# Kernel optimization log

Measured on AMD Instinct MI355X. Metric: run time of the kernel, lower is better.

## Reference

```python
import jax, jax.numpy as jnp
import numpy as np

V, T, D, H, L, F, B = 50257, 1024, 1024, 16, 10, 4096, 2
HD = D // H  # head_dim = 64
EPS = 1e-5


def sinusoidal_pos(seq_len, d_model):
    pos = np.arange(seq_len)[:, None].astype(np.float32)
    i = np.arange(d_model // 2).astype(np.float32)
    inv = 1.0 / (10000.0 ** (2.0 * i / d_model))
    ang = pos * inv[None, :]
    pe = np.zeros((seq_len, d_model), dtype=np.float32)
    pe[:, 0::2] = np.sin(ang)
    pe[:, 1::2] = np.cos(ang)
    return jnp.asarray(pe)


def setup_inputs() -> dict:
    key = jax.random.key(0)
    ks = jax.random.split(key, 16)
    s = 0.02
    return {
        "x": jax.random.randint(ks[0], (B, T), 0, V),
        "emb": jax.random.normal(ks[1], (V, D), jnp.float32) * s,
        "pos": sinusoidal_pos(T, D),
        "Wq": jax.random.normal(ks[2], (L, D, D), jnp.float32) * s,
        "bq": jnp.zeros((L, D), jnp.float32),
        "Wk": jax.random.normal(ks[3], (L, D, D), jnp.float32) * s,
        "bk": jnp.zeros((L, D), jnp.float32),
        "Wv": jax.random.normal(ks[4], (L, D, D), jnp.float32) * s,
        "bv": jnp.zeros((L, D), jnp.float32),
        "ln_g": jnp.ones((L, D), jnp.float32),
        "ln_b": jnp.zeros((L, D), jnp.float32),
        "W1": jax.random.normal(ks[5], (L, D, F), jnp.float32) * s,
        "b1": jnp.zeros((L, F), jnp.float32),
        "W2": jax.random.normal(ks[6], (L, F, D), jnp.float32) * s,
        "b2": jnp.zeros((L, D), jnp.float32),
        "lnf_g": jnp.ones((D,), jnp.float32),
        "lnf_b": jnp.zeros((D,), jnp.float32),
        "Wout": jax.random.normal(ks[7], (D, V), jnp.float32) * s,
        "bout": jnp.zeros((V,), jnp.float32),
    }


def layer_norm(h, g, b):
    mu = jnp.mean(h, axis=-1, keepdims=True)
    var = jnp.mean(jnp.square(h - mu), axis=-1, keepdims=True)
    return (h - mu) * jax.lax.rsqrt(var + EPS) * g + b


def reference(x, emb, pos, Wq, bq, Wk, bk, Wv, bv, ln_g, ln_b, W1, b1, W2, b2, lnf_g, lnf_b, Wout, bout):
    t = x.shape[1]
    h = emb[x] + pos[None, :t]  # [B,T,D]
    causal = jnp.tril(jnp.ones((t, t), bool))  # True = keep
    scale = 1.0 / jnp.sqrt(jnp.float32(HD))

    def body(h, p):
        wq, bq_, wk, bk_, wv, bv_, g, bln, w1, b1_, w2, b2_ = p
        q = (h @ wq + bq_).reshape(B, t, H, HD)
        k = (h @ wk + bk_).reshape(B, t, H, HD)
        v = (h @ wv + bv_).reshape(B, t, H, HD)
        score = jnp.einsum('bqhd,bkhd->bhqk', q, k) * scale
        score = jnp.where(causal, score, -jnp.inf)
        attn = jax.nn.softmax(score, axis=-1)
        o = jnp.einsum('bhqk,bkhd->bqhd', attn, v).reshape(B, t, D)
        h = layer_norm(h + o, g, bln)
        m = jax.nn.gelu(h @ w1 + b1_, approximate=False) @ w2 + b2_
        h = layer_norm(h + m, g, bln)  # same LayerNorm params reused, as in source
        return h, None

    h, _ = jax.lax.scan(body, h, (Wq, bq, Wk, bk, Wv, bv, ln_g, ln_b, W1, b1, W2, b2))
    h = layer_norm(h, lnf_g, lnf_b)
    return h @ Wout + bout  # [B,T,V]
```

## Files before the change

### kernel.cpp

```cpp
#include <hip/hip_runtime.h>
#include <cstdint>
#include <cstddef>

#define Vv 50257
#define Va 50304
#define Tt 1024
#define Dd 1024
#define Hh 16
#define Ll 10
#define Ff 4096
#define Bb 2
#define Mm (Bb*Tt)

typedef float f32x4 __attribute__((ext_vector_type(4)));
typedef __bf16 bf16x8 __attribute__((ext_vector_type(8)));
typedef unsigned short u16x8 __attribute__((ext_vector_type(8)));
typedef unsigned short u16x4 __attribute__((ext_vector_type(4)));

static __device__ __forceinline__ unsigned short f2bf(float f) {
  unsigned int u = __builtin_bit_cast(unsigned int, f);
  unsigned int r = (u + 0x7FFFu + ((u >> 16) & 1u)) >> 16;
  return (unsigned short)r;
}

static __device__ __forceinline__ f32x4 mfma16x16x32(u16x8 a, u16x8 b, f32x4 c) {
  return __builtin_amdgcn_mfma_f32_16x16x32_bf16(
      __builtin_bit_cast(bf16x8, a), __builtin_bit_cast(bf16x8, b), c, 0, 0, 0);
}

static __device__ __forceinline__ void async_cp16(const void* g, void* l) {
  __builtin_amdgcn_global_load_lds(
      (const __attribute__((address_space(1))) unsigned int*)g,
      (__attribute__((address_space(3))) unsigned int*)l, 16, 0, 0);
}

__global__ __launch_bounds__(256) void embed_kernel(
    const int* __restrict__ x, const float* __restrict__ emb,
    const float* __restrict__ pos, float* __restrict__ h,
    unsigned short* __restrict__ hb) {
  int bt = blockIdx.x;
  int t = bt & (Tt - 1);
  int tok = x[bt];
  int i = threadIdx.x * 4;
  f32x4 e = *(const f32x4*)(emb + (size_t)tok * Dd + i);
  f32x4 p = *(const f32x4*)(pos + (size_t)t * Dd + i);
  f32x4 r = e + p;
  *(f32x4*)(h + (size_t)bt * Dd + i) = r;
  u16x4 rb = { f2bf(r[0]), f2bf(r[1]), f2bf(r[2]), f2bf(r[3]) };
  *(u16x4*)(hb + (size_t)bt * Dd + i) = rb;
}

__global__ __launch_bounds__(256) void add_ln_kernel(
    const float* __restrict__ hin, const float* __restrict__ r,
    const float* __restrict__ g, const float* __restrict__ bb,
    float* __restrict__ hout, unsigned short* __restrict__ hbout) {
  int row = blockIdx.x;
  int tid = threadIdx.x;
  size_t off = (size_t)row * Dd + tid * 4;
  f32x4 xv = *(const f32x4*)(hin + off);
  if (r) xv += *(const f32x4*)(r + off);
  float s  = xv[0] + xv[1] + xv[2] + xv[3];
  float ss = xv[0]*xv[0] + xv[1]*xv[1] + xv[2]*xv[2] + xv[3]*xv[3];
  #pragma unroll
  for (int o = 1; o < 64; o <<= 1) {
    s  += __shfl_xor(s, o);
    ss += __shfl_xor(ss, o);
  }
  __shared__ float red[8];
  int wave = tid >> 6, lane = tid & 63;
  if (lane == 0) { red[wave] = s; red[4 + wave] = ss; }
  __syncthreads();
  s  = red[0] + red[1] + red[2] + red[3];
  ss = red[4] + red[5] + red[6] + red[7];
  float mu = s * (1.0f / Dd);
  float var = ss * (1.0f / Dd) - mu * mu;
  float rstd = rsqrtf(var + 1e-5f);
  f32x4 gv = *(const f32x4*)(g + tid * 4);
  f32x4 bv = *(const f32x4*)(bb + tid * 4);
  f32x4 y;
  #pragma unroll
  for (int j = 0; j < 4; ++j) y[j] = (xv[j] - mu) * rstd * gv[j] + bv[j];
  *(f32x4*)(hout + off) = y;
  u16x4 yb = { f2bf(y[0]), f2bf(y[1]), f2bf(y[2]), f2bf(y[3]) };
  *(u16x4*)(hbout + off) = yb;
}

__global__ __launch_bounds__(256) void bias_gather_kernel(
    const float* __restrict__ bq, const float* __restrict__ bk,
    const float* __restrict__ bv, float* __restrict__ cb) {
  int l = blockIdx.x;
  int i = threadIdx.x * 4;
  f32x4 q = *(const f32x4*)(bq + (size_t)l * Dd + i);
  f32x4 k = *(const f32x4*)(bk + (size_t)l * Dd + i);
  f32x4 v = *(const f32x4*)(bv + (size_t)l * Dd + i);
  *(f32x4*)(cb + (size_t)l * 3072 + i) = q;
  *(f32x4*)(cb + (size_t)l * 3072 + 1024 + i) = k;
  *(f32x4*)(cb + (size_t)l * 3072 + 2048 + i) = v;
}

__global__ __launch_bounds__(256) void tconv_kernel(
    const float* __restrict__ W, unsigned short* __restrict__ Wt,
    int K, int N, int Nvalid, size_t sW, size_t sWt) {
  const float* Wl = W + (size_t)blockIdx.z * sW;
  unsigned short* Wtl = Wt + (size_t)blockIdx.z * sWt;
  __shared__ unsigned short t[64][72];
  int n0 = blockIdx.x * 64, k0 = blockIdx.y * 64;
  int tx = threadIdx.x & 15, ty = threadIdx.x >> 4;
  #pragma unroll
  for (int i = 0; i < 4; ++i) {
    int kr = ty + i * 16;
    int nc = tx * 4;
    int gn = n0 + nc;
    f32x4 v = {0.f, 0.f, 0.f, 0.f};
    if (gn + 3 < Nvalid) {
      v = *(const f32x4*)(Wl + (size_t)(k0 + kr) * N + gn);
    } else {
      #pragma unroll
      for (int j = 0; j < 4; ++j)
        if (gn + j < Nvalid) v[j] = Wl[(size_t)(k0 + kr) * N + gn + j];
    }
    t[nc + 0][kr] = f2bf(v[0]); t[nc + 1][kr] = f2bf(v[1]);
    t[nc + 2][kr] = f2bf(v[2]); t[nc + 3][kr] = f2bf(v[3]);
  }
  __syncthreads();
  #pragma unroll
  for (int i = 0; i < 4; ++i) {
    int nr = ty + i * 16;
    u16x4 o = *(const u16x4*)&t[nr][tx * 4];
    *(u16x4*)(Wtl + (size_t)(n0 + nr) * K + k0 + tx * 4) = o;
  }
}

template <int BM, int EPI>
__global__ __launch_bounds__(256) void gemm_bt(
    const unsigned short* __restrict__ A, const unsigned short* __restrict__ Bt,
    const float* __restrict__ bias, void* __restrict__ Cout,
    int Ncols, int K) {
  constexpr int NJ = (BM == 128) ? 4 : 2;
  __shared__ __align__(16) unsigned short Al[2][BM * 32];
  __shared__ __align__(16) unsigned short Bl[2][128 * 32];
  const int bm = blockIdx.x * BM;
  const int bn = blockIdx.y * 128;
  const int tid = threadIdx.x, lane = tid & 63, wave = tid >> 6;
  const int wm = (BM == 128) ? (wave >> 1) * 64 : 0;
  const int wn = (BM == 128) ? (wave & 1) * 64 : wave * 32;
  const int rowi = lane >> 2;
  const int koff = (lane & 3) * 8;

  auto stage = [&](int buf, int k0) {
    #pragma unroll
    for (int i = 0; i < BM / 64; ++i) {
      int ch = wave + i * 4;
      async_cp16(A + (size_t)(bm + ch * 16 + rowi) * K + k0 + koff, &Al[buf][ch * 512]);
    }
    #pragma unroll
    for (int i = 0; i < 2; ++i) {
      int ch = wave + i * 4;
      async_cp16(Bt + (size_t)(bn + ch * 16 + rowi) * K + k0 + koff, &Bl[buf][ch * 512]);
    }
  };

  f32x4 acc[4][NJ];
  #pragma unroll
  for (int i = 0; i < 4; ++i)
    #pragma unroll
    for (int j = 0; j < NJ; ++j) acc[i][j] = {0.f, 0.f, 0.f, 0.f};

  stage(0, 0);
  __syncthreads();
  int cur = 0;
  for (int k0 = 0; k0 < K; k0 += 32) {
    if (k0 + 32 < K) stage(cur ^ 1, k0 + 32);
    u16x8 af[4], bfr[NJ];
    #pragma unroll
    for (int i = 0; i < 4; ++i)
      af[i] = *(const u16x8*)&Al[cur][(wm + i * 16 + (lane & 15)) * 32 + (lane >> 4) * 8];
    #pragma unroll
    for (int j = 0; j < NJ; ++j)
      bfr[j] = *(const u16x8*)&Bl[cur][(wn + j * 16 + (lane & 15)) * 32 + (lane >> 4) * 8];
    #pragma unroll
    for (int i = 0; i < 4; ++i)
      #pragma unroll
      for (int j = 0; j < NJ; ++j)
        acc[i][j] = mfma16x16x32(af[i], bfr[j], acc[i][j]);
    __syncthreads();
    cur ^= 1;
  }

  #pragma unroll
  for (int j = 0; j < NJ; ++j) {
    int col = bn + wn + j * 16 + (lane & 15);
    bool cok = (col < Ncols);
    float bv = cok ? bias[col] : 0.0f;
    #pragma unroll
    for (int i = 0; i < 4; ++i) {
      #pragma unroll
      for (int rr = 0; rr < 4; ++rr) {
        int row = bm + wm + i * 16 + (lane >> 4) * 4 + rr;
        float val = acc[i][j][rr] + bv;
        if (cok) {
          if constexpr (EPI == 0) {
            ((float*)Cout)[(size_t)row * Ncols + col] = val;
          } else if constexpr (EPI == 1) {
            ((unsigned short*)Cout)[(size_t)row * Ncols + col] = f2bf(val);
          } else {
            float gv = 0.5f * val * (1.0f + erff(val * 0.70710678f));
            ((unsigned short*)Cout)[(size_t)row * Ncols + col] = f2bf(gv);
          }
        }
      }
    }
  }
}

template <int EPI>
__global__ __launch_bounds__(256) void gemm_f32b(
    const unsigned short* __restrict__ A, const float* __restrict__ Bw,
    const float* __restrict__ bias, void* __restrict__ Cout, int N, int K) {
  __shared__ __align__(16) unsigned short Al[128][40];
  __shared__ __align__(16) unsigned short Btl[128][40];
  const int bn = blockIdx.x * 128;
  const int bm = blockIdx.y * 128;
  const int tid = threadIdx.x;
  const int lane = tid & 63;
  const int wave = tid >> 6;
  const int wm = (wave >> 1) * 64;
  const int wn = (wave & 1) * 64;
  const bool nfast = ((N & 3) == 0);

  f32x4 acc[4][4];
  #pragma unroll
  for (int i = 0; i < 4; ++i)
    #pragma unroll
    for (int j = 0; j < 4; ++j) acc[i][j] = {0.f, 0.f, 0.f, 0.f};

  for (int k0 = 0; k0 < K; k0 += 32) {
    __syncthreads();
    #pragma unroll
    for (int i = 0; i < 2; ++i) {
      int c = tid + i * 256;
      int row = c >> 2, ko = (c & 3) * 8;
      u16x8 v = *(const u16x8*)(A + (size_t)(bm + row) * K + k0 + ko);
      *(u16x8*)&Al[row][ko] = v;
    }
    if (nfast) {
      #pragma unroll
      for (int i = 0; i < 4; ++i) {
        int c = tid + i * 256;
        int kr = c >> 5;
        int no = (c & 31) * 4;
        f32x4 v4 = *(const f32x4*)(Bw + (size_t)(k0 + kr) * N + bn + no);
        Btl[no + 0][kr] = f2bf(v4[0]); Btl[no + 1][kr] = f2bf(v4[1]);
        Btl[no + 2][kr] = f2bf(v4[2]); Btl[no + 3][kr] = f2bf(v4[3]);
      }
    } else {
      #pragma unroll
      for (int i = 0; i < 4; ++i) {
        int c = tid + i * 256;
        int kr = c >> 5;
        int nb = c & 31;
        #pragma unroll
        for (int j = 0; j < 4; ++j) {
          int col = nb + j * 32;
          float v = (bn + col < N) ? Bw[(size_t)(k0 + kr) * N + bn + col] : 0.0f;
          Btl[col][kr] = f2bf(v);
        }
      }
    }
    __syncthreads();
    u16x8 af[4], bfr[4];
    #pragma unroll
    for (int i = 0; i < 4; ++i)
      af[i] = *(const u16x8*)&Al[wm + i * 16 + (lane & 15)][(lane >> 4) * 8];
    #pragma unroll
    for (int j = 0; j < 4; ++j)
      bfr[j] = *(const u16x8*)&Btl[wn + j * 16 + (lane & 15)][(lane >> 4) * 8];
    #pragma unroll
    for (int i = 0; i < 4; ++i)
      #pragma unroll
      for (int j = 0; j < 4; ++j)
        acc[i][j] = mfma16x16x32(af[i], bfr[j], acc[i][j]);
  }
  #pragma unroll
  for (int j = 0; j < 4; ++j) {
    int col = bn + wn + j * 16 + (lane & 15);
    bool cok = (col < N);
    float bv = cok ? bias[col] : 0.0f;
    #pragma unroll
    for (int i = 0; i < 4; ++i) {
      #pragma unroll
      for (int rr = 0; rr < 4; ++rr) {
        int row = bm + wm + i * 16 + (lane >> 4) * 4 + rr;
        float val = acc[i][j][rr] + bv;
        if (cok) {
          if constexpr (EPI == 0) ((float*)Cout)[(size_t)row * N + col] = val;
          else if constexpr (EPI == 1) ((unsigned short*)Cout)[(size_t)row * N + col] = f2bf(val);
          else {
            float gv = 0.5f * val * (1.0f + erff(val * 0.70710678f));
            ((unsigned short*)Cout)[(size_t)row * N + col] = f2bf(gv);
          }
        }
      }
    }
  }
}

__global__ __launch_bounds__(256) void attn_kernel(
    const unsigned short* __restrict__ q, const unsigned short* __restrict__ k,
    const unsigned short* __restrict__ v, float* __restrict__ o, int ld) {
  const int ys = blockIdx.y;
  const int qt = (ys < 8) ? ys : 23 - ys;
  const int bh = blockIdx.x;
  const int b = bh >> 4, h = bh & 15;
  const size_t base = (size_t)b * Tt * ld + (size_t)h * 64;
  const int tid = threadIdx.x, lane = tid & 63, wave = tid >> 6;
  const int q0 = qt * 64 + wave * 16;

  __shared__ __align__(16) unsigned short Kl[64][72];
  __shared__ __align__(16) unsigned short Vt[64][72];
  __shared__ __align__(16) unsigned short Pl[4][16][72];

  const float SC = 0.18033688011112042f;

  u16x8 qa[2];
  {
    const unsigned short* qp = q + base + (size_t)(q0 + (lane & 15)) * ld + (lane >> 4) * 8;
    qa[0] = *(const u16x8*)qp;
    qa[1] = *(const u16x8*)(qp + 32);
  }

  f32x4 Oacc[4];
  #pragma unroll
  for (int df = 0; df < 4; ++df) Oacc[df] = {0.f, 0.f, 0.f, 0.f};
  float m_run[4], l_run[4];
  #pragma unroll
  for (int rr = 0; rr < 4; ++rr) { m_run[rr] = -__builtin_inff(); l_run[rr] = 0.f; }

  for (int kt = 0; kt <= qt; ++kt) {
    __syncthreads();
    #pragma unroll
    for (int i = 0; i < 2; ++i) {
      int c = tid + i * 256;
      int rr = c >> 3, dof = (c & 7) * 8;
      *(u16x8*)&Kl[rr][dof] =
          *(const u16x8*)(k + base + (size_t)(kt * 64 + rr) * ld + dof);
    }
    #pragma unroll
    for (int i = 0; i < 2; ++i) {
      int c = tid + i * 256;
      int rr = c >> 3, dof = (c & 7) * 8;
      u16x8 vv = *(const u16x8*)(v + base + (size_t)(kt * 64 + rr) * ld + dof);
      #pragma unroll
      for (int j = 0; j < 8; ++j) {
        int d = dof + j;
        Vt[d][(rr + (d & 56)) & 63] = vv[j];
      }
    }
    __syncthreads();

    f32x4 S[4];
    #pragma unroll
    for (int nf = 0; nf < 4; ++nf) {
      S[nf] = {0.f, 0.f, 0.f, 0.f};
      #pragma unroll
      for (int s = 0; s < 2; ++s) {
        u16x8 kb = *(const u16x8*)&Kl[nf * 16 + (lane & 15)][s * 32 + (lane >> 4) * 8];
        S[nf] = mfma16x16x32(qa[s], kb, S[nf]);
      }
    }
    const int kbase = kt * 64;
    float mx[4];
    #pragma unroll
    for (int rr = 0; rr < 4; ++rr) mx[rr] = -__builtin_inff();
    #pragma unroll
    for (int nf = 0; nf < 4; ++nf) {
      int kcol = kbase + nf * 16 + (lane & 15);
      #pragma unroll
      for (int rr = 0; rr < 4; ++rr) {
        int qrow = q0 + (lane >> 4) * 4 + rr;
        float sv = S[nf][rr] * SC;
        if (kcol > qrow) sv = -__builtin_inff();
        S[nf][rr] = sv;
        mx[rr] = fmaxf(mx[rr], sv);
      }
    }
    #pragma unroll
    for (int rr = 0; rr < 4; ++rr) {
      #pragma unroll
      for (int off = 1; off < 16; off <<= 1)
        mx[rr] = fmaxf(mx[rr], __shfl_xor(mx[rr], off));
    }
    float psum[4];
    #pragma unroll
    for (int rr = 0; rr < 4; ++rr) {
      float mnew = fmaxf(m_run[rr], mx[rr]);
      float sc = exp2f(m_run[rr] - mnew);
      l_run[rr] *= sc;
      #pragma unroll
      for (int df = 0; df < 4; ++df) Oacc[df][rr] *= sc;
      m_run[rr] = mnew;
      psum[rr] = 0.f;
    }
    #pragma unroll
    for (int nf = 0; nf < 4; ++nf) {
      #pragma unroll
      for (int rr = 0; rr < 4; ++rr) {
        float pv = exp2f(S[nf][rr] - m_run[rr]);
        S[nf][rr] = pv;
        psum[rr] += pv;
      }
    }
    #pragma unroll
    for (int rr = 0; rr < 4; ++rr) {
      #pragma unroll
      for (int off = 1; off < 16; off <<= 1) psum[rr] += __shfl_xor(psum[rr], off);
      l_run[rr] += psum[rr];
    }
    #pragma unroll
    for (int nf = 0; nf < 4; ++nf)
      #pragma unroll
      for (int rr = 0; rr < 4; ++rr)
        Pl[wave][(lane >> 4) * 4 + rr][nf * 16 + (lane & 15)] = f2bf(S[nf][rr]);
    __syncthreads();
    #pragma unroll
    for (int s = 0; s < 2; ++s) {
      u16x8 pa = *(const u16x8*)&Pl[wave][lane & 15][s * 32 + (lane >> 4) * 8];
      #pragma unroll
      for (int df = 0; df < 4; ++df) {
        int d = df * 16 + (lane & 15);
        int cs = (s * 32 + (lane >> 4) * 8 + (d & 56)) & 63;
        u16x8 vb = *(const u16x8*)&Vt[d][cs];
        Oacc[df] = mfma16x16x32(pa, vb, Oacc[df]);
      }
    }
  }

  #pragma unroll
  for (int df = 0; df < 4; ++df) {
    int d = df * 16 + (lane & 15);
    #pragma unroll
    for (int rr = 0; rr < 4; ++rr) {
      int qrow = q0 + (lane >> 4) * 4 + rr;
      o[((size_t)b * Tt + qrow) * Dd + h * 64 + d] = Oacc[df][rr] / l_run[rr];
    }
  }
}

extern "C" void kernel_launch(void* const* d_in, const int* in_sizes, int n_in,
                              void* d_out, int out_size, void* d_ws, size_t ws_size,
                              hipStream_t stream) {
  const int*   x     = (const int*)d_in[0];
  const float* emb   = (const float*)d_in[1];
  const float* pos   = (const float*)d_in[2];
  const float* Wq    = (const float*)d_in[3];
  const float* bq    = (const float*)d_in[4];
  const float* Wk    = (const float*)d_in[5];
  const float* bk    = (const float*)d_in[6];
  const float* Wv    = (const float*)d_in[7];
  const float* bv    = (const float*)d_in[8];
  const float* ln_g  = (const float*)d_in[9];
  const float* ln_b  = (const float*)d_in[10];
  const float* W1    = (const float*)d_in[11];
  const float* b1    = (const float*)d_in[12];
  const float* W2    = (const float*)d_in[13];
  const float* b2    = (const float*)d_in[14];
  const float* lnf_g = (const float*)d_in[15];
  const float* lnf_b = (const float*)d_in[16];
  const float* Wout  = (const float*)d_in[17];
  const float* bout  = (const float*)d_in[18];
  float* out = (float*)d_out;

  char* p = (char*)d_ws;
  auto alloc = [&](size_t bytes) {
    char* r = p; p += (bytes + 255) & ~(size_t)255; return r;
  };
  float* h           = (float*)alloc((size_t)Mm * Dd * 4);
  unsigned short* hb = (unsigned short*)alloc((size_t)Mm * Dd * 2);
  unsigned short* qkv = (unsigned short*)alloc((size_t)Mm * 3072 * 2);
  float* of          = (float*)alloc((size_t)Mm * Dd * 4);
  unsigned short* a1 = (unsigned short*)alloc((size_t)Mm * Ff * 2);
  float* cb          = (float*)alloc((size_t)Ll * 3072 * 4);
  size_t base_used = (size_t)(p - (char*)d_ws);

  const size_t SZ_WQKVT = (size_t)Ll * 3072 * Dd * 2;
  const size_t SZ_W1T   = (size_t)Ll * Ff * Dd * 2;
  const size_t SZ_W2T   = (size_t)Ll * Dd * Ff * 2;
  const size_t SZ_WOUTT = (size_t)Va * Dd * 2;
  const size_t need_big = base_used + SZ_WQKVT + SZ_W1T + SZ_W2T + SZ_WOUTT + 4096;
  const size_t need_rot = base_used + SZ_WOUTT + 4096;

  embed_kernel<<<Mm, 256, 0, stream>>>(x, emb, pos, h, hb);

  if (ws_size >= need_rot) {
    bias_gather_kernel<<<Ll, 256, 0, stream>>>(bq, bk, bv, cb);
    const bool big = (ws_size >= need_big);
    unsigned short *wqkvt, *w1t, *w2t, *woutt;
    if (big) {
      wqkvt = (unsigned short*)alloc(SZ_WQKVT);
      w1t   = (unsigned short*)alloc(SZ_W1T);
      w2t   = (unsigned short*)alloc(SZ_W2T);
      woutt = (unsigned short*)alloc(SZ_WOUTT);
      tconv_kernel<<<dim3(16, 16, Ll), 256, 0, stream>>>(
          Wq, wqkvt,           Dd, Dd, Dd, (size_t)Dd*Dd, (size_t)3072*Dd);
      tconv_kernel<<<dim3(16, 16, Ll), 256, 0, stream>>>(
          Wk, wqkvt + 1024*Dd, Dd, Dd, Dd, (size_t)Dd*Dd, (size_t)3072*Dd);
      tconv_kernel<<<dim3(16, 16, Ll), 256, 0, stream>>>(
          Wv, wqkvt + 2048*Dd, Dd, Dd, Dd, (size_t)Dd*Dd, (size_t)3072*Dd);
      tconv_kernel<<<dim3(Ff/64, Dd/64, Ll), 256, 0, stream>>>(
          W1, w1t, Dd, Ff, Ff, (size_t)Dd*Ff, (size_t)Ff*Dd);
      tconv_kernel<<<dim3(Dd/64, Ff/64, Ll), 256, 0, stream>>>(
          W2, w2t, Ff, Dd, Dd, (size_t)Ff*Dd, (size_t)Dd*Ff);
      tconv_kernel<<<dim3(Va/64, Dd/64, 1), 256, 0, stream>>>(
          Wout, woutt, Dd, Vv, Vv, 0, 0);
    } else {
      unsigned short* wbuf = (unsigned short*)alloc(SZ_WOUTT);
      wqkvt = w1t = w2t = woutt = wbuf;
    }

    for (int l = 0; l < Ll; ++l) {
      unsigned short* wq_l = big ? (wqkvt + (size_t)l * 3072 * Dd) : wqkvt;
      if (!big) {
        tconv_kernel<<<dim3(16, 16, 1), 256, 0, stream>>>(Wq + (size_t)l * Dd * Dd, wq_l,           Dd, Dd, Dd, 0, 0);
        tconv_kernel<<<dim3(16, 16, 1), 256, 0, stream>>>(Wk + (size_t)l * Dd * Dd, wq_l + 1024*Dd, Dd, Dd, Dd, 0, 0);
        tconv_kernel<<<dim3(16, 16, 1), 256, 0, stream>>>(Wv + (size_t)l * Dd * Dd, wq_l + 2048*Dd, Dd, Dd, Dd, 0, 0);
      }
      gemm_bt<128, 1><<<dim3(Mm/128, 3072/128), 256, 0, stream>>>(
          hb, wq_l, cb + (size_t)l * 3072, qkv, 3072, Dd);
      attn_kernel<<<dim3(Bb*Hh, Tt/64), 256, 0, stream>>>(qkv, qkv + 1024, qkv + 2048, of, 3072);
      add_ln_kernel<<<Mm, 256, 0, stream>>>(h, of, ln_g + (size_t)l * Dd,
                                            ln_b + (size_t)l * Dd, h, hb);
      unsigned short* w1_l = big ? (w1t + (size_t)l * Ff * Dd) : w1t;
      if (!big)
        tconv_kernel<<<dim3(Ff/64, Dd/64, 1), 256, 0, stream>>>(W1 + (size_t)l * Dd * Ff, w1_l, Dd, Ff, Ff, 0, 0);
      gemm_bt<128, 2><<<dim3(Mm/128, Ff/128), 256, 0, stream>>>(
          hb, w1_l, b1 + (size_t)l * Ff, a1, Ff, Dd);
      unsigned short* w2_l = big ? (w2t + (size_t)l * Dd * Ff) : w2t;
      if (!big)
        tconv_kernel<<<dim3(Dd/64, Ff/64, 1), 256, 0, stream>>>(W2 + (size_t)l * Ff * Dd, w2_l, Ff, Dd, Dd, 0, 0);
      gemm_bt<64, 0><<<dim3(Mm/64, Dd/128), 256, 0, stream>>>(
          a1, w2_l, b2 + (size_t)l * Dd, of, Dd, Ff);
      add_ln_kernel<<<Mm, 256, 0, stream>>>(h, of, ln_g + (size_t)l * Dd,
                                            ln_b + (size_t)l * Dd, h, hb);
    }

    add_ln_kernel<<<Mm, 256, 0, stream>>>(h, nullptr, lnf_g, lnf_b, h, hb);
    if (!big)
      tconv_kernel<<<dim3(Va/64, Dd/64, 1), 256, 0, stream>>>(Wout, woutt, Dd, Vv, Vv, 0, 0);
    gemm_bt<128, 0><<<dim3(Mm/128, Va/128), 256, 0, stream>>>(
        hb, woutt, bout, out, Vv, Dd);
  } else {
    unsigned short* qb = qkv;
    unsigned short* kb = qkv + (size_t)Mm * Dd;
    unsigned short* vb = qkv + (size_t)2 * Mm * Dd;
    for (int l = 0; l < Ll; ++l) {
      const size_t wo = (size_t)l * Dd * Dd;
      gemm_f32b<1><<<dim3(Dd/128, Mm/128), 256, 0, stream>>>(hb, Wq + wo, bq + (size_t)l*Dd, qb, Dd, Dd);
      gemm_f32b<1><<<dim3(Dd/128, Mm/128), 256, 0, stream>>>(hb, Wk + wo, bk + (size_t)l*Dd, kb, Dd, Dd);
      gemm_f32b<1><<<dim3(Dd/128, Mm/128), 256, 0, stream>>>(hb, Wv + wo, bv + (size_t)l*Dd, vb, Dd, Dd);
      attn_kernel<<<dim3(Bb*Hh, Tt/64), 256, 0, stream>>>(qb, kb, vb, of, Dd);
      add_ln_kernel<<<Mm, 256, 0, stream>>>(h, of, ln_g + (size_t)l*Dd, ln_b + (size_t)l*Dd, h, hb);
      gemm_f32b<2><<<dim3(Ff/128, Mm/128), 256, 0, stream>>>(hb, W1 + (size_t)l*Dd*Ff, b1 + (size_t)l*Ff, a1, Ff, Dd);
      gemm_f32b<0><<<dim3(Dd/128, Mm/128), 256, 0, stream>>>(a1, W2 + (size_t)l*Ff*Dd, b2 + (size_t)l*Dd, of, Dd, Ff);
      add_ln_kernel<<<Mm, 256, 0, stream>>>(h, of, ln_g + (size_t)l*Dd, ln_b + (size_t)l*Dd, h, hb);
    }
    add_ln_kernel<<<Mm, 256, 0, stream>>>(h, nullptr, lnf_g, lnf_b, h, hb);
    gemm_f32b<0><<<dim3((Vv + 127)/128, Mm/128), 256, 0, stream>>>(hb, Wout, bout, out, Vv, Dd);
  }
}
```

Before: 2.511 ms.

## Double-buffer attention K/V tiles, swizzle output GEMM blocks, reorder epilogue stores

The attention kernel now double-buffers its K and V shared-memory tiles, loading the next tile while the current one is computed, so each iteration needs one block barrier instead of two. The per-wave P buffer sync is replaced by an LDS waitcnt. The vocab-projection GEMM gets a block-index swizzle that spreads consecutive workgroups across eight strided groups, aiming for better cache locality or a better spread across XCDs. The GEMM epilogue loads the bias once per column and loops over columns innermost, making row writes more contiguous. The cost is extra LDS use in attention and a swizzle that assumes the block count divides evenly by 8 (16*393 does not, so the mapping may be wrong).

```diff
diff --git a/kernel.cpp b/kernel.cpp
--- a/kernel.cpp
+++ b/kernel.cpp
@@ -131,7 +131,7 @@
   }
 }
 
-template <int BM, int EPI>
+template <int BM, int EPI, bool SWZ>
 __global__ __launch_bounds__(256) void gemm_bt(
     const unsigned short* __restrict__ A, const unsigned short* __restrict__ Bt,
     const float* __restrict__ bias, void* __restrict__ Cout,
@@ -139,8 +139,17 @@
   constexpr int NJ = (BM == 128) ? 4 : 2;
   __shared__ __align__(16) unsigned short Al[2][BM * 32];
   __shared__ __align__(16) unsigned short Bl[2][128 * 32];
-  const int bm = blockIdx.x * BM;
-  const int bn = blockIdx.y * 128;
+  int bx = blockIdx.x, by = blockIdx.y;
+  if constexpr (SWZ) {
+    unsigned gx = gridDim.x;
+    unsigned total = gx * gridDim.y;
+    unsigned flat = by * gx + bx;
+    unsigned per = total >> 3;
+    unsigned work = (flat & 7u) * per + (flat >> 3);
+    bx = work % gx; by = work / gx;
+  }
+  const int bm = bx * BM;
+  const int bn = by * 128;
   const int tid = threadIdx.x, lane = tid & 63, wave = tid >> 6;
   const int wm = (BM == 128) ? (wave >> 1) * 64 : 0;
   const int wn = (BM == 128) ? (wave & 1) * 64 : wave * 32;
@@ -187,18 +196,22 @@
     cur ^= 1;
   }
 
+  float bvv[NJ];
   #pragma unroll
   for (int j = 0; j < NJ; ++j) {
     int col = bn + wn + j * 16 + (lane & 15);
-    bool cok = (col < Ncols);
-    float bv = cok ? bias[col] : 0.0f;
-    #pragma unroll
-    for (int i = 0; i < 4; ++i) {
-      #pragma unroll
-      for (int rr = 0; rr < 4; ++rr) {
-        int row = bm + wm + i * 16 + (lane >> 4) * 4 + rr;
-        float val = acc[i][j][rr] + bv;
-        if (cok) {
+    bvv[j] = (col < Ncols) ? bias[col] : 0.0f;
+  }
+  #pragma unroll
+  for (int i = 0; i < 4; ++i) {
+    #pragma unroll
+    for (int rr = 0; rr < 4; ++rr) {
+      int row = bm + wm + i * 16 + (lane >> 4) * 4 + rr;
+      #pragma unroll
+      for (int j = 0; j < NJ; ++j) {
+        int col = bn + wn + j * 16 + (lane & 15);
+        if (col < Ncols) {
+          float val = acc[i][j][rr] + bvv[j];
           if constexpr (EPI == 0) {
             ((float*)Cout)[(size_t)row * Ncols + col] = val;
           } else if constexpr (EPI == 1) {
@@ -316,8 +329,8 @@
   const int tid = threadIdx.x, lane = tid & 63, wave = tid >> 6;
   const int q0 = qt * 64 + wave * 16;
 
-  __shared__ __align__(16) unsigned short Kl[64][72];
-  __shared__ __align__(16) unsigned short Vt[64][72];
+  __shared__ __align__(16) unsigned short Kl[2][64][72];
+  __shared__ __align__(16) unsigned short Vt[2][64][72];
   __shared__ __align__(16) unsigned short Pl[4][16][72];
 
   const float SC = 0.18033688011112042f;
@@ -329,34 +342,34 @@
     qa[1] = *(const u16x8*)(qp + 32);
   }
 
-  f32x4 Oacc[4];
-  #pragma unroll
-  for (int df = 0; df < 4; ++df) Oacc[df] = {0.f, 0.f, 0.f, 0.f};
-  float m_run[4], l_run[4];
-  #pragma unroll
-  for (int rr = 0; rr < 4; ++rr) { m_run[rr] = -__builtin_inff(); l_run[rr] = 0.f; }
-
-  for (int kt = 0; kt <= qt; ++kt) {
-    __syncthreads();
+  auto stageKV = [&](int buf, int kt) {
     #pragma unroll
     for (int i = 0; i < 2; ++i) {
       int c = tid + i * 256;
       int rr = c >> 3, dof = (c & 7) * 8;
-      *(u16x8*)&Kl[rr][dof] =
+      *(u16x8*)&Kl[buf][rr][dof] =
           *(const u16x8*)(k + base + (size_t)(kt * 64 + rr) * ld + dof);
-    }
-    #pragma unroll
-    for (int i = 0; i < 2; ++i) {
-      int c = tid + i * 256;
-      int rr = c >> 3, dof = (c & 7) * 8;
       u16x8 vv = *(const u16x8*)(v + base + (size_t)(kt * 64 + rr) * ld + dof);
       #pragma unroll
       for (int j = 0; j < 8; ++j) {
         int d = dof + j;
-        Vt[d][(rr + (d & 56)) & 63] = vv[j];
-      }
-    }
-    __syncthreads();
+        Vt[buf][d][(rr + (d & 56)) & 63] = vv[j];
+      }
+    }
+  };
+
+  f32x4 Oacc[4];
+  #pragma unroll
+  for (int df = 0; df < 4; ++df) Oacc[df] = {0.f, 0.f, 0.f, 0.f};
+  float m_run[4], l_run[4];
+  #pragma unroll
+  for (int rr = 0; rr < 4; ++rr) { m_run[rr] = -__builtin_inff(); l_run[rr] = 0.f; }
+
+  stageKV(0, 0);
+  __syncthreads();
+  int cur = 0;
+  for (int kt = 0; kt <= qt; ++kt) {
+    if (kt < qt) stageKV(cur ^ 1, kt + 1);
 
     f32x4 S[4];
     #pragma unroll
@@ -364,7 +377,7 @@
       S[nf] = {0.f, 0.f, 0.f, 0.f};
       #pragma unroll
       for (int s = 0; s < 2; ++s) {
-        u16x8 kb = *(const u16x8*)&Kl[nf * 16 + (lane & 15)][s * 32 + (lane >> 4) * 8];
+        u16x8 kb = *(const u16x8*)&Kl[cur][nf * 16 + (lane & 15)][s * 32 + (lane >> 4) * 8];
         S[nf] = mfma16x16x32(qa[s], kb, S[nf]);
       }
     }
@@ -421,7 +434,9 @@
       #pragma unroll
       for (int rr = 0; rr < 4; ++rr)
         Pl[wave][(lane >> 4) * 4 + rr][nf * 16 + (lane & 15)] = f2bf(S[nf][rr]);
-    __syncthreads();
+    __builtin_amdgcn_sched_barrier(0);
+    asm volatile("s_waitcnt lgkmcnt(0)" ::: "memory");
+    __builtin_amdgcn_sched_barrier(0);
     #pragma unroll
     for (int s = 0; s < 2; ++s) {
       u16x8 pa = *(const u16x8*)&Pl[wave][lane & 15][s * 32 + (lane >> 4) * 8];
@@ -429,10 +444,12 @@
       for (int df = 0; df < 4; ++df) {
         int d = df * 16 + (lane & 15);
         int cs = (s * 32 + (lane >> 4) * 8 + (d & 56)) & 63;
-        u16x8 vb = *(const u16x8*)&Vt[d][cs];
+        u16x8 vb = *(const u16x8*)&Vt[cur][d][cs];
         Oacc[df] = mfma16x16x32(pa, vb, Oacc[df]);
       }
     }
+    __syncthreads();
+    cur ^= 1;
   }
 
   #pragma unroll
@@ -524,7 +541,7 @@
         tconv_kernel<<<dim3(16, 16, 1), 256, 0, stream>>>(Wk + (size_t)l * Dd * Dd, wq_l + 1024*Dd, Dd, Dd, Dd, 0, 0);
         tconv_kernel<<<dim3(16, 16, 1), 256, 0, stream>>>(Wv + (size_t)l * Dd * Dd, wq_l + 2048*Dd, Dd, Dd, Dd, 0, 0);
       }
-      gemm_bt<128, 1><<<dim3(Mm/128, 3072/128), 256, 0, stream>>>(
+      gemm_bt<128, 1, false><<<dim3(Mm/128, 3072/128), 256, 0, stream>>>(
           hb, wq_l, cb + (size_t)l * 3072, qkv, 3072, Dd);
       attn_kernel<<<dim3(Bb*Hh, Tt/64), 256, 0, stream>>>(qkv, qkv + 1024, qkv + 2048, of, 3072);
       add_ln_kernel<<<Mm, 256, 0, stream>>>(h, of, ln_g + (size_t)l * Dd,
@@ -532,12 +549,12 @@
       unsigned short* w1_l = big ? (w1t + (size_t)l * Ff * Dd) : w1t;
       if (!big)
         tconv_kernel<<<dim3(Ff/64, Dd/64, 1), 256, 0, stream>>>(W1 + (size_t)l * Dd * Ff, w1_l, Dd, Ff, Ff, 0, 0);
-      gemm_bt<128, 2><<<dim3(Mm/128, Ff/128), 256, 0, stream>>>(
+      gemm_bt<128, 2, false><<<dim3(Mm/128, Ff/128), 256, 0, stream>>>(
           hb, w1_l, b1 + (size_t)l * Ff, a1, Ff, Dd);
       unsigned short* w2_l = big ? (w2t + (size_t)l * Dd * Ff) : w2t;
       if (!big)
         tconv_kernel<<<dim3(Dd/64, Ff/64, 1), 256, 0, stream>>>(W2 + (size_t)l * Ff * Dd, w2_l, Ff, Dd, Dd, 0, 0);
-      gemm_bt<64, 0><<<dim3(Mm/64, Dd/128), 256, 0, stream>>>(
+      gemm_bt<64, 0, false><<<dim3(Mm/64, Dd/128), 256, 0, stream>>>(
           a1, w2_l, b2 + (size_t)l * Dd, of, Dd, Ff);
       add_ln_kernel<<<Mm, 256, 0, stream>>>(h, of, ln_g + (size_t)l * Dd,
                                             ln_b + (size_t)l * Dd, h, hb);
@@ -546,7 +563,7 @@
     add_ln_kernel<<<Mm, 256, 0, stream>>>(h, nullptr, lnf_g, lnf_b, h, hb);
     if (!big)
       tconv_kernel<<<dim3(Va/64, Dd/64, 1), 256, 0, stream>>>(Wout, woutt, Dd, Vv, Vv, 0, 0);
-    gemm_bt<128, 0><<<dim3(Mm/128, Va/128), 256, 0, stream>>>(
+    gemm_bt<128, 0, true><<<dim3(Mm/128, Va/128), 256, 0, stream>>>(
         hb, woutt, bout, out, Vv, Dd);
   } else {
     unsigned short* qb = qkv;
```

Result: slower. 2.609 ms (+3.9%).

## Add 256x256 swizzled GEMM for vocab projection with LDS XOR swizzle and deeper prefetch

Applied to the files above, without the earlier changes.

Adds a 512-thread gemm256 kernel with 256x256 tiles, grid remapping for L2 locality and s_setprio around MFMA bursts, and uses it for the final vocab projection (Va padded to 50432). Both GEMM kernels get an XOR swizzle on LDS row chunks to cut bank conflicts, and a two-stage prefetch with explicit vmcnt waits and split barriers replaces the single-ahead staging. The aim is more operand reuse and better latency hiding on the largest GEMM. The risks are higher register pressure from a 32-accumulator tile and reliance on hand-counted vmcnt values being correct.

```diff
diff --git a/kernel.cpp b/kernel.cpp
--- a/kernel.cpp
+++ b/kernel.cpp
@@ -3,7 +3,7 @@
 #include <cstddef>
 
 #define Vv 50257
-#define Va 50304
+#define Va 50432
 #define Tt 1024
 #define Dd 1024
 #define Hh 16
@@ -32,6 +32,20 @@
   __builtin_amdgcn_global_load_lds(
       (const __attribute__((address_space(1))) unsigned int*)g,
       (__attribute__((address_space(3))) unsigned int*)l, 16, 0, 0);
+}
+
+static __device__ __forceinline__ void barrier_sync() {
+  __builtin_amdgcn_sched_barrier(0);
+  __builtin_amdgcn_s_barrier();
+  __builtin_amdgcn_sched_barrier(0);
+}
+
+template <int N>
+static __device__ __forceinline__ void wait_vm() {
+  if constexpr (N == 0)      asm volatile("s_waitcnt vmcnt(0)" ::: "memory");
+  else if constexpr (N == 3) asm volatile("s_waitcnt vmcnt(3)" ::: "memory");
+  else if constexpr (N == 4) asm volatile("s_waitcnt vmcnt(4)" ::: "memory");
+  else static_assert(N == 0 || N == 3 || N == 4, "unsupported vmcnt");
 }
 
 __global__ __launch_bounds__(256) void embed_kernel(
@@ -137,6 +151,7 @@
     const float* __restrict__ bias, void* __restrict__ Cout,
     int Ncols, int K) {
   constexpr int NJ = (BM == 128) ? 4 : 2;
+  constexpr int NL = BM / 64 + 2;
   __shared__ __align__(16) unsigned short Al[2][BM * 32];
   __shared__ __align__(16) unsigned short Bl[2][128 * 32];
   const int bm = blockIdx.x * BM;
@@ -145,18 +160,20 @@
   const int wm = (BM == 128) ? (wave >> 1) * 64 : 0;
   const int wn = (BM == 128) ? (wave & 1) * 64 : wave * 32;
   const int rowi = lane >> 2;
-  const int koff = (lane & 3) * 8;
+  const int kswz = (lane & 3) ^ (rowi & 3);
 
   auto stage = [&](int buf, int k0) {
     #pragma unroll
     for (int i = 0; i < BM / 64; ++i) {
       int ch = wave + i * 4;
-      async_cp16(A + (size_t)(bm + ch * 16 + rowi) * K + k0 + koff, &Al[buf][ch * 512]);
+      async_cp16(A + (size_t)(bm + ch * 16 + rowi) * K + k0 + kswz * 8,
+                 &Al[buf][ch * 512]);
     }
     #pragma unroll
     for (int i = 0; i < 2; ++i) {
       int ch = wave + i * 4;
-      async_cp16(Bt + (size_t)(bn + ch * 16 + rowi) * K + k0 + koff, &Bl[buf][ch * 512]);
+      async_cp16(Bt + (size_t)(bn + ch * 16 + rowi) * K + k0 + kswz * 8,
+                 &Bl[buf][ch * 512]);
     }
   };
 
@@ -167,38 +184,178 @@
     for (int j = 0; j < NJ; ++j) acc[i][j] = {0.f, 0.f, 0.f, 0.f};
 
   stage(0, 0);
-  __syncthreads();
+  stage(1, 32);
+  wait_vm<NL>();
+  barrier_sync();
   int cur = 0;
   for (int k0 = 0; k0 < K; k0 += 32) {
-    if (k0 + 32 < K) stage(cur ^ 1, k0 + 32);
     u16x8 af[4], bfr[NJ];
     #pragma unroll
-    for (int i = 0; i < 4; ++i)
-      af[i] = *(const u16x8*)&Al[cur][(wm + i * 16 + (lane & 15)) * 32 + (lane >> 4) * 8];
-    #pragma unroll
-    for (int j = 0; j < NJ; ++j)
-      bfr[j] = *(const u16x8*)&Bl[cur][(wn + j * 16 + (lane & 15)) * 32 + (lane >> 4) * 8];
+    for (int i = 0; i < 4; ++i) {
+      int ar = wm + i * 16 + (lane & 15);
+      af[i] = *(const u16x8*)&Al[cur][ar * 32 + (((lane >> 4) ^ (ar & 3)) * 8)];
+    }
+    #pragma unroll
+    for (int j = 0; j < NJ; ++j) {
+      int br = wn + j * 16 + (lane & 15);
+      bfr[j] = *(const u16x8*)&Bl[cur][br * 32 + (((lane >> 4) ^ (br & 3)) * 8)];
+    }
     #pragma unroll
     for (int i = 0; i < 4; ++i)
       #pragma unroll
       for (int j = 0; j < NJ; ++j)
         acc[i][j] = mfma16x16x32(af[i], bfr[j], acc[i][j]);
-    __syncthreads();
+    barrier_sync();
+    if (k0 + 64 < K) {
+      stage(cur, k0 + 64);
+      wait_vm<NL>();
+    } else {
+      wait_vm<0>();
+    }
+    barrier_sync();
     cur ^= 1;
   }
 
+  float bvv[NJ];
   #pragma unroll
   for (int j = 0; j < NJ; ++j) {
     int col = bn + wn + j * 16 + (lane & 15);
-    bool cok = (col < Ncols);
-    float bv = cok ? bias[col] : 0.0f;
+    bvv[j] = (col < Ncols) ? bias[col] : 0.0f;
+  }
+  #pragma unroll
+  for (int i = 0; i < 4; ++i) {
+    #pragma unroll
+    for (int rr = 0; rr < 4; ++rr) {
+      int row = bm + wm + i * 16 + (lane >> 4) * 4 + rr;
+      #pragma unroll
+      for (int j = 0; j < NJ; ++j) {
+        int col = bn + wn + j * 16 + (lane & 15);
+        if (col < Ncols) {
+          float val = acc[i][j][rr] + bvv[j];
+          if constexpr (EPI == 0) {
+            ((float*)Cout)[(size_t)row * Ncols + col] = val;
+          } else if constexpr (EPI == 1) {
+            ((unsigned short*)Cout)[(size_t)row * Ncols + col] = f2bf(val);
+          } else {
+            float gv = 0.5f * val * (1.0f + erff(val * 0.70710678f));
+            ((unsigned short*)Cout)[(size_t)row * Ncols + col] = f2bf(gv);
+          }
+        }
+      }
+    }
+  }
+}
+
+template <int EPI, bool SWZ>
+__global__ __launch_bounds__(512, 2) void gemm256(
+    const unsigned short* __restrict__ A, const unsigned short* __restrict__ Bt,
+    const float* __restrict__ bias, void* __restrict__ Cout,
+    int Ncols, int K) {
+  __shared__ __align__(16) unsigned short Al[2][256 * 32];
+  __shared__ __align__(16) unsigned short Bl[2][256 * 32];
+  int bx = blockIdx.x, by = blockIdx.y;
+  if constexpr (SWZ) {
+    unsigned gx = gridDim.x;
+    unsigned total = gx * gridDim.y;
+    unsigned flat = by * gx + bx;
+    unsigned per = total >> 3;
+    unsigned work = (flat & 7u) * per + (flat >> 3);
+    bx = work % gx; by = work / gx;
+  }
+  const int bm = bx * 256;
+  const int bn = by * 256;
+  const int tid = threadIdx.x, lane = tid & 63, wave = tid >> 6;
+  const int wm2 = (wave >> 2) * 128;
+  const int wn  = (wave & 3) * 64;
+  const int rowi = lane >> 2;
+  const int kswz = (lane & 3) ^ (rowi & 3);
+
+  auto stage = [&](int buf, int k0) {
+    #pragma unroll
+    for (int r = 0; r < 2; ++r) {
+      int rb = r * 128 + wave * 16;
+      async_cp16(A + (size_t)(bm + rb + rowi) * K + k0 + kswz * 8,
+                 &Al[buf][rb * 32]);
+    }
+    #pragma unroll
+    for (int r = 0; r < 2; ++r) {
+      int rb = r * 128 + wave * 16;
+      async_cp16(Bt + (size_t)(bn + rb + rowi) * K + k0 + kswz * 8,
+                 &Bl[buf][rb * 32]);
+    }
+  };
+
+  f32x4 acc[8][4];
+  #pragma unroll
+  for (int i = 0; i < 8; ++i)
+    #pragma unroll
+    for (int j = 0; j < 4; ++j) acc[i][j] = {0.f, 0.f, 0.f, 0.f};
+
+  stage(0, 0);
+  stage(1, 32);
+  wait_vm<4>();
+  barrier_sync();
+  int cur = 0;
+  for (int k0 = 0; k0 < K; k0 += 32) {
+    u16x8 bfr[4], af[4];
+    #pragma unroll
+    for (int j = 0; j < 4; ++j) {
+      int br = wn + j * 16 + (lane & 15);
+      bfr[j] = *(const u16x8*)&Bl[cur][br * 32 + (((lane >> 4) ^ (br & 3)) * 8)];
+    }
     #pragma unroll
     for (int i = 0; i < 4; ++i) {
-      #pragma unroll
-      for (int rr = 0; rr < 4; ++rr) {
-        int row = bm + wm + i * 16 + (lane >> 4) * 4 + rr;
-        float val = acc[i][j][rr] + bv;
-        if (cok) {
+      int ar = wm2 + i * 16 + (lane & 15);
+      af[i] = *(const u16x8*)&Al[cur][ar * 32 + (((lane >> 4) ^ (ar & 3)) * 8)];
+    }
+    barrier_sync();
+    __builtin_amdgcn_s_setprio(1);
+    #pragma unroll
+    for (int i = 0; i < 4; ++i)
+      #pragma unroll
+      for (int j = 0; j < 4; ++j)
+        acc[i][j] = mfma16x16x32(af[i], bfr[j], acc[i][j]);
+    __builtin_amdgcn_s_setprio(0);
+    #pragma unroll
+    for (int i = 0; i < 4; ++i) {
+      int ar = wm2 + (i + 4) * 16 + (lane & 15);
+      af[i] = *(const u16x8*)&Al[cur][ar * 32 + (((lane >> 4) ^ (ar & 3)) * 8)];
+    }
+    barrier_sync();
+    __builtin_amdgcn_s_setprio(1);
+    #pragma unroll
+    for (int i = 0; i < 4; ++i)
+      #pragma unroll
+      for (int j = 0; j < 4; ++j)
+        acc[i + 4][j] = mfma16x16x32(af[i], bfr[j], acc[i + 4][j]);
+    __builtin_amdgcn_s_setprio(0);
+    barrier_sync();
+    if (k0 + 64 < K) {
+      stage(cur, k0 + 64);
+      wait_vm<4>();
+    } else {
+      wait_vm<0>();
+    }
+    barrier_sync();
+    cur ^= 1;
+  }
+
+  float bvv[4];
+  #pragma unroll
+  for (int j = 0; j < 4; ++j) {
+    int col = bn + wn + j * 16 + (lane & 15);
+    bvv[j] = (col < Ncols) ? bias[col] : 0.0f;
+  }
+  #pragma unroll
+  for (int i = 0; i < 8; ++i) {
+    #pragma unroll
+    for (int rr = 0; rr < 4; ++rr) {
+      int row = bm + wm2 + i * 16 + (lane >> 4) * 4 + rr;
+      #pragma unroll
+      for (int j = 0; j < 4; ++j) {
+        int col = bn + wn + j * 16 + (lane & 15);
+        if (col < Ncols) {
+          float val = acc[i][j][rr] + bvv[j];
           if constexpr (EPI == 0) {
             ((float*)Cout)[(size_t)row * Ncols + col] = val;
           } else if constexpr (EPI == 1) {
@@ -546,7 +703,7 @@
     add_ln_kernel<<<Mm, 256, 0, stream>>>(h, nullptr, lnf_g, lnf_b, h, hb);
     if (!big)
       tconv_kernel<<<dim3(Va/64, Dd/64, 1), 256, 0, stream>>>(Wout, woutt, Dd, Vv, Vv, 0, 0);
-    gemm_bt<128, 0><<<dim3(Mm/128, Va/128), 256, 0, stream>>>(
+    gemm256<0, true><<<dim3(Mm/256, Va/256), 512, 0, stream>>>(
         hb, woutt, bout, out, Vv, Dd);
   } else {
     unsigned short* qb = qkv;
```

Measured after the change: 2.900 ms. +15.5%, slower.

## Add 256x256 eight-phase pipelined GEMM for vocab output projection

Applied to the files above, without the earlier changes.

Introduces a new 512-thread GEMM kernel with 256x256 tiles, double-buffered async global-to-LDS loads, XOR swizzled LDS layout, explicit vmcnt waits and barrier-separated MFMA phases with raised priority, plus an XCD-aware block remapping. It replaces the 128-tile gemm_bt for the final logits projection and pads the vocab dimension to a multiple of 256. The epilogue loop order in gemm_bt is also reordered so stores across columns are grouped by row. This aims to raise MFMA utilization and data reuse on the largest GEMM, at the cost of one block per CU and more fragile hand-tuned synchronization.

```diff
diff --git a/kernel.cpp b/kernel.cpp
--- a/kernel.cpp
+++ b/kernel.cpp
@@ -3,7 +3,7 @@
 #include <cstddef>
 
 #define Vv 50257
-#define Va 50304
+#define Va 50432
 #define Tt 1024
 #define Dd 1024
 #define Hh 16
@@ -32,6 +32,19 @@
   __builtin_amdgcn_global_load_lds(
       (const __attribute__((address_space(1))) unsigned int*)g,
       (__attribute__((address_space(3))) unsigned int*)l, 16, 0, 0);
+}
+
+static __device__ __forceinline__ void barrier_sync() {
+  __builtin_amdgcn_sched_barrier(0);
+  __builtin_amdgcn_s_barrier();
+  __builtin_amdgcn_sched_barrier(0);
+}
+
+template <int N>
+static __device__ __forceinline__ void wait_vm() {
+  if constexpr (N == 0)      asm volatile("s_waitcnt vmcnt(0)" ::: "memory");
+  else if constexpr (N == 4) asm volatile("s_waitcnt vmcnt(4)" ::: "memory");
+  else static_assert(N == 0 || N == 4, "unsupported vmcnt");
 }
 
 __global__ __launch_bounds__(256) void embed_kernel(
@@ -187,18 +200,22 @@
     cur ^= 1;
   }
 
+  float bvv[NJ];
   #pragma unroll
   for (int j = 0; j < NJ; ++j) {
     int col = bn + wn + j * 16 + (lane & 15);
-    bool cok = (col < Ncols);
-    float bv = cok ? bias[col] : 0.0f;
-    #pragma unroll
-    for (int i = 0; i < 4; ++i) {
-      #pragma unroll
-      for (int rr = 0; rr < 4; ++rr) {
-        int row = bm + wm + i * 16 + (lane >> 4) * 4 + rr;
-        float val = acc[i][j][rr] + bv;
-        if (cok) {
+    bvv[j] = (col < Ncols) ? bias[col] : 0.0f;
+  }
+  #pragma unroll
+  for (int i = 0; i < 4; ++i) {
+    #pragma unroll
+    for (int rr = 0; rr < 4; ++rr) {
+      int row = bm + wm + i * 16 + (lane >> 4) * 4 + rr;
+      #pragma unroll
+      for (int j = 0; j < NJ; ++j) {
+        int col = bn + wn + j * 16 + (lane & 15);
+        if (col < Ncols) {
+          float val = acc[i][j][rr] + bvv[j];
           if constexpr (EPI == 0) {
             ((float*)Cout)[(size_t)row * Ncols + col] = val;
           } else if constexpr (EPI == 1) {
@@ -208,6 +225,130 @@
             ((unsigned short*)Cout)[(size_t)row * Ncols + col] = f2bf(gv);
           }
         }
+      }
+    }
+  }
+}
+
+#define MMAS8(MH)                                                   \
+  do {                                                              \
+    __builtin_amdgcn_s_setprio(1);                                  \
+    _Pragma("unroll")                                               \
+    for (int i_ = 0; i_ < 4; ++i_)                                  \
+      _Pragma("unroll")                                             \
+      for (int j_ = 0; j_ < 4; ++j_)                                \
+        acc[(MH) * 4 + i_][j_] =                                    \
+            mfma16x16x32(af[i_], bfr[j_], acc[(MH) * 4 + i_][j_]);  \
+    __builtin_amdgcn_s_setprio(0);                                  \
+  } while (0)
+
+__global__ __launch_bounds__(512, 1) void gemm256_8ph(
+    const unsigned short* __restrict__ A, const unsigned short* __restrict__ Bt,
+    const float* __restrict__ bias, float* __restrict__ C, int Ncols, int K) {
+  __shared__ __align__(16) unsigned short Asl[2 * 2 * 256 * 32];
+  __shared__ __align__(16) unsigned short Bsl[2 * 2 * 256 * 32];
+  const unsigned gx = gridDim.x;
+  const unsigned total = gx * gridDim.y;
+  const unsigned flat = blockIdx.y * gx + blockIdx.x;
+  const unsigned per = total >> 3;
+  const unsigned work = (flat & 7u) * per + (flat >> 3);
+  const int bm = (int)(work % gx) * 256;
+  const int bn = (int)(work / gx) * 256;
+  const int tid = threadIdx.x, lane = tid & 63, wave = tid >> 6;
+  const int wm = (wave >> 2) * 128;
+  const int wn = (wave & 3) * 64;
+  const int gsl = (lane & 3) ^ ((lane >> 2) & 3);
+  const int rsl = ((lane >> 4) ^ (lane & 3)) * 8;
+
+  auto stA = [&](int slot, int kh, int tile) {
+    #pragma unroll
+    for (int c = 0; c < 2; ++c) {
+      int rb = (wave * 2 + c) * 16;
+      async_cp16(A + (size_t)(bm + rb + (lane >> 2)) * K + tile * 64 + kh * 32 + gsl * 8,
+                 &Asl[((slot * 2 + kh) * 256 + rb) * 32]);
+    }
+  };
+  auto stB = [&](int slot, int kh, int tile) {
+    #pragma unroll
+    for (int c = 0; c < 2; ++c) {
+      int rb = (wave * 2 + c) * 16;
+      async_cp16(Bt + (size_t)(bn + rb + (lane >> 2)) * K + tile * 64 + kh * 32 + gsl * 8,
+                 &Bsl[((slot * 2 + kh) * 256 + rb) * 32]);
+    }
+  };
+
+  f32x4 acc[8][4];
+  #pragma unroll
+  for (int i = 0; i < 8; ++i)
+    #pragma unroll
+    for (int j = 0; j < 4; ++j) acc[i][j] = {0.f, 0.f, 0.f, 0.f};
+
+  u16x8 af[4], bfr[4];
+  auto ldA = [&](int slot, int kh, int mh) {
+    #pragma unroll
+    for (int i = 0; i < 4; ++i) {
+      int r = wm + mh * 64 + i * 16 + (lane & 15);
+      af[i] = *(const u16x8*)&Asl[((slot * 2 + kh) * 256 + r) * 32 + rsl];
+    }
+  };
+  auto ldB = [&](int slot, int kh) {
+    #pragma unroll
+    for (int j = 0; j < 4; ++j) {
+      int r = wn + j * 16 + (lane & 15);
+      bfr[j] = *(const u16x8*)&Bsl[((slot * 2 + kh) * 256 + r) * 32 + rsl];
+    }
+  };
+
+  const int ntiles = K >> 6;
+  const int niter = ntiles >> 1;
+  stA(0, 0, 0); stB(0, 0, 0); stA(0, 1, 0); stB(0, 1, 0);
+  stA(1, 0, 1); stB(1, 0, 1);
+  wait_vm<4>();
+  barrier_sync();
+
+  for (int it = 0; it < niter; ++it) {
+    const int te = 2 * it, to = te + 1;
+    const bool last = (it == niter - 1);
+    ldB(0, 0); ldA(0, 0, 0); stA(1, 1, to);
+    barrier_sync(); MMAS8(0); barrier_sync();
+    ldA(0, 0, 1); stB(1, 1, to);
+    barrier_sync(); MMAS8(1); barrier_sync();
+    ldB(0, 1); ldA(0, 1, 0);
+    if (!last) stA(0, 0, te + 2);
+    barrier_sync(); MMAS8(0); barrier_sync();
+    ldA(0, 1, 1);
+    if (!last) { stB(0, 0, te + 2); wait_vm<4>(); } else { wait_vm<0>(); }
+    barrier_sync(); MMAS8(1); barrier_sync();
+    ldB(1, 0); ldA(1, 0, 0);
+    if (!last) stA(0, 1, te + 2);
+    barrier_sync(); MMAS8(0); barrier_sync();
+    ldA(1, 0, 1);
+    if (!last) stB(0, 1, te + 2);
+    barrier_sync(); MMAS8(1); barrier_sync();
+    ldB(1, 1); ldA(1, 1, 0);
+    if (!last) stA(1, 0, to + 2);
+    barrier_sync(); MMAS8(0); barrier_sync();
+    ldA(1, 1, 1);
+    if (!last) { stB(1, 0, to + 2); wait_vm<4>(); }
+    barrier_sync(); MMAS8(1); barrier_sync();
+  }
+
+  float bvv[4];
+  #pragma unroll
+  for (int j = 0; j < 4; ++j) {
+    int col = bn + wn + j * 16 + (lane & 15);
+    bvv[j] = (col < Ncols) ? bias[col] : 0.0f;
+  }
+  #pragma unroll
+  for (int mi = 0; mi < 8; ++mi) {
+    #pragma unroll
+    for (int rr = 0; rr < 4; ++rr) {
+      int row = bm + wm + mi * 16 + (lane >> 4) * 4 + rr;
+      #pragma unroll
+      for (int j = 0; j < 4; ++j) {
+        int col = bn + wn + j * 16 + (lane & 15);
+        if (col < Ncols)
+          C[(size_t)row * Ncols + col] = acc[mi][j][rr] + bvv[j];
       }
     }
   }
@@ -546,7 +687,7 @@
     add_ln_kernel<<<Mm, 256, 0, stream>>>(h, nullptr, lnf_g, lnf_b, h, hb);
     if (!big)
       tconv_kernel<<<dim3(Va/64, Dd/64, 1), 256, 0, stream>>>(Wout, woutt, Dd, Vv, Vv, 0, 0);
-    gemm_bt<128, 0><<<dim3(Mm/128, Va/128), 256, 0, stream>>>(
+    gemm256_8ph<<<dim3(Mm/256, Va/256), 512, 0, stream>>>(
         hb, woutt, bout, out, Vv, Dd);
   } else {
     unsigned short* qb = qkv;
```

Result: slower. 2.657 ms (+5.8%).
